# Kernel tuning notes

Measured on AMD Instinct MI355X. Metric: run time of the kernel, lower is better.

## Reference

```python
import jax, jax.numpy as jnp
from jax import lax
import numpy as np

S, B, HP, WP, CIN, CO, DS, DI, K = 6, 1, 37, 37, 1536, 256, 16, 512, 4
N = HP * WP          # 1369 patches (37x37 grid)
OH, OW = 148, 148
HID = max(S * CO // 4, S)  # 384, attention hidden


def setup_inputs() -> dict:
    key = jax.random.key(0)
    ks = iter(jax.random.split(key, 64))
    def nrm(shape, scale):
        return jax.random.normal(next(ks), shape, jnp.float32) * scale
    inp = {}
    inp["features"] = nrm((S, B, 1, N, CIN), 1.0)
    # AdaptiveFusionModule (global branch)
    inp["proj_w"] = nrm((S, CO, CIN), CIN ** -0.5)          # per-source 1x1 conv
    inp["attn_w1"] = nrm((S * CO, HID), (S * CO) ** -0.5)
    inp["attn_b1"] = jnp.zeros((HID,), jnp.float32)
    inp["attn_w2"] = nrm((HID, S), HID ** -0.5)
    inp["attn_b2"] = jnp.zeros((S,), jnp.float32)
    inp["src_scale"] = jnp.ones((S,), jnp.float32)
    # two SelectiveSSM parameter sets (fwd / bwd scan)
    def ssm_params(tag):
        d = {}
        d[tag + "_in_w"] = nrm((CO, 2 * DI), CO ** -0.5)
        d[tag + "_conv_w"] = nrm((K, DI), K ** -0.5)         # depthwise causal conv
        d[tag + "_conv_b"] = jnp.zeros((DI,), jnp.float32)
        d[tag + "_xp_w"] = nrm((DI, 2 * DS + DI + 1), 0.02)  # B, C, delta, dt_bias
        # trained A_log; scaled so the log-domain cumsum stays in fp32 range over L=1369
        d[tag + "_Alog"] = jnp.log(jnp.arange(1, DS + 1, dtype=jnp.float32) / 1000.0) * jnp.ones((DI, 1), jnp.float32)
        d[tag + "_D"] = jnp.ones((DI,), jnp.float32)
        d[tag + "_out_w"] = nrm((DI, CO), DI ** -0.5)
        d[tag + "_ln_g"] = jnp.ones((CO,), jnp.float32)
        d[tag + "_ln_b"] = jnp.zeros((CO,), jnp.float32)
        return d
    inp.update(ssm_params("f"))
    inp.update(ssm_params("b"))
    inp["merge_w"] = nrm((2 * CO, CO), (2 * CO) ** -0.5)     # MSSR merge 1x1 conv
    inp["co1_w"] = nrm((3, 3, CO, CO), (9 * CO) ** -0.5)     # conv_out1, HWIO
    inp["co1_b"] = jnp.zeros((CO,), jnp.float32)
    inp["hp"], inp["wp"], inp["out_h"], inp["out_w"] = HP, WP, OH, OW
    return inp


def _causal_dwconv(z, w, b):
    # z: [B,L,D], w: [K,D] -> torch Conv1d(groups=D, padding=K-1)[..., :L]
    Kk, L = w.shape[0], z.shape[1]
    zp = jnp.pad(z, ((0, 0), (Kk - 1, 0), (0, 0)))
    return sum(zp[:, k:k + L, :] * w[k] for k in range(Kk)) + b


def _ssm(x, in_w, conv_w, conv_b, xp_w, Alog, D, out_w, ln_g, ln_b):
    # x: [B,L,d_model] -> [B,L,d_model]
    z, gate = jnp.split(x @ in_w, 2, axis=-1)               # [B,L,DI] each
    z = jax.nn.silu(_causal_dwconv(z, conv_w, conv_b))
    xp = z @ xp_w                                           # [B,L,2*DS+DI+1]
    ds = Alog.shape[1]
    Bp, Cp = xp[..., :ds], xp[..., ds:2 * ds]
    delta = jax.nn.softplus(xp[..., 2 * ds:-1] + xp[..., -1:])  # [B,L,DI]
    dA = jnp.exp(delta[..., None] * (-jnp.exp(Alog)))       # [B,L,DI,DS]
    dBu = delta[..., None] * Bp[:, :, None, :] * z[..., None]
    # log-domain cumsum scan: h[t] = sum_s exp(cs[t]-cs[s]) * dBu[s]
    cs = jnp.cumsum(jnp.log(jnp.clip(dA, 1e-38)), axis=1)
    h = jnp.exp(cs) * jnp.cumsum(jnp.exp(-cs) * dBu, axis=1)
    y = (h * Cp[:, :, None, :]).sum(-1) + D * z             # [B,L,DI]
    y = (y * jax.nn.silu(gate)) @ out_w                     # [B,L,d_model]
    r = y + x                                               # residual + LayerNorm
    mu = r.mean(-1, keepdims=True)
    v = ((r - mu) ** 2).mean(-1, keepdims=True)
    return ln_g * (r - mu) * lax.rsqrt(v + 1e-5) + ln_b


def _forward(features, proj_w, attn_w1, attn_b1, attn_w2, attn_b2, src_scale,
             f_in_w, f_conv_w, f_conv_b, f_xp_w, f_Alog, f_D, f_out_w, f_ln_g, f_ln_b,
             b_in_w, b_conv_w, b_conv_b, b_xp_w, b_Alog, b_D, b_out_w, b_ln_g, b_ln_b,
             merge_w, co1_w, co1_b, hp, wp, out_h, out_w):
    feats = features[:, :, 0]                               # [S,B,N,Cin]
    pf = jnp.einsum('sbnc,soc->sbno', feats, proj_w)        # [S,B,N,Co] per-source 1x1 proj
    Bsz = pf.shape[1]
    concat = pf.mean(2).transpose(1, 0, 2).reshape(Bsz, -1)  # [B,S*Co] pooled concat
    w = jax.nn.softmax(jax.nn.relu(concat @ attn_w1 + attn_b1) @ attn_w2 + attn_b2, axis=-1)
    w = jax.nn.softmax(w * src_scale, axis=-1)              # double softmax as in torch
    fused = jnp.einsum('bs,sbnc->bnc', w, pf)               # [B,N,Co]
    # MSSR bidirectional scan over row-major flattened patches
    fwd = _ssm(fused, f_in_w, f_conv_w, f_conv_b, f_xp_w, f_Alog, f_D, f_out_w, f_ln_g, f_ln_b)
    bwd = _ssm(fused[:, ::-1], b_in_w, b_conv_w, b_conv_b, b_xp_w, b_Alog, b_D, b_out_w, b_ln_g, b_ln_b)[:, ::-1]
    out = jnp.concatenate([fwd, bwd], axis=-1) @ merge_w    # [B,N,Co]
    sp = out.reshape(Bsz, hp, wp, -1)                       # NHWC
    up = jax.image.resize(sp, (Bsz, out_h, out_w, sp.shape[-1]), method='bilinear')
    y = lax.conv_general_dilated(up, co1_w, (1, 1), 'SAME',
                                 dimension_numbers=('NHWC', 'HWIO', 'NHWC')) + co1_b
    return y.transpose(0, 3, 1, 2)                          # [B,Co,out_h,out_w]


def reference(features, proj_w, attn_w1, attn_b1, attn_w2, attn_b2, src_scale,
              f_in_w, f_conv_w, f_conv_b, f_xp_w, f_Alog, f_D, f_out_w, f_ln_g, f_ln_b,
              b_in_w, b_conv_w, b_conv_b, b_xp_w, b_Alog, b_D, b_out_w, b_ln_g, b_ln_b,
              merge_w, co1_w, co1_b, hp, wp, out_h, out_w):
    return _forward(features, proj_w, attn_w1, attn_b1, attn_w2, attn_b2, src_scale,
                    f_in_w, f_conv_w, f_conv_b, f_xp_w, f_Alog, f_D, f_out_w, f_ln_g, f_ln_b,
                    b_in_w, b_conv_w, b_conv_b, b_xp_w, b_Alog, b_D, b_out_w, b_ln_g, b_ln_b,
                    merge_w, co1_w, co1_b, hp, wp, out_h, out_w)
```

## Files before the change

### kernel.cpp

```cpp
#include <hip/hip_runtime.h>
#include <math.h>


namespace {
constexpr int kS   = 6;
constexpr int kHP  = 37;
constexpr int kWP  = 37;
constexpr int kN   = 1369;
constexpr int kCIN = 1536;
constexpr int kCO  = 256;
constexpr int kDS  = 16;
constexpr int kDI  = 512;
constexpr int kHID = 384;
constexpr int kOH  = 148;
constexpr int kOW  = 148;
constexpr int kNP  = kOH * kOW;
constexpr int kXPW = 545;
constexpr long kXPS = 746112;
constexpr int kNC  = 24;
constexpr int kCH  = 58;

constexpr long OFF_PF      = 0;
constexpr long OFF_Z2B     = 0;
constexpr long OFF_YGB     = 0;
constexpr long OFF_UPB     = 0;
constexpr long OFF_SCANP   = 700928;
constexpr long OFF_SCANH   = 1094144;
constexpr long OFF_HIN     = 1487360;
constexpr long OFF_OUTWT   = 1880576;
constexpr long OFF_COLPART = 2102784;
constexpr long OFF_WFIN    = 2119680;
constexpr long OFF_ATTNP   = 2119696;
constexpr long OFF_INWT    = 2200000;
constexpr long OFF_FUSEDB  = 2462144;
constexpr long OFF_ZG      = 2820624;
constexpr long OFF_Z       = 5760000;
constexpr long OFF_WCONVB  = 6000000;
constexpr long OFF_XP      = 7161856;
constexpr long OFF_DELTA   = 8654080;
constexpr long OFF_Y       = 10055936;
constexpr long OFF_GT      = 11457792;
constexpr long OFF_XPWT    = 11457792;
constexpr long OFF_FUSED2  = 12158720;
constexpr long OFF_CAT     = 12859648;
constexpr long OFF_MERGEWT = 13210112;
constexpr long OFF_MERGED  = 13560576;
}

typedef __attribute__((ext_vector_type(8))) short bf16x8;
typedef __attribute__((ext_vector_type(4))) float f32x4;

__device__ __forceinline__ short f2bf(float x) {
    unsigned u = __builtin_bit_cast(unsigned, x);
    unsigned r = u + 0x7fffu + ((u >> 16) & 1u);
    return (short)(r >> 16);
}

__device__ __forceinline__ bf16x8 cvt8(float4 x, float4 y) {
    union { short s[8]; bf16x8 v; } u;
    u.s[0] = f2bf(x.x); u.s[1] = f2bf(x.y); u.s[2] = f2bf(x.z); u.s[3] = f2bf(x.w);
    u.s[4] = f2bf(y.x); u.s[5] = f2bf(y.y); u.s[6] = f2bf(y.z); u.s[7] = f2bf(y.w);
    return u.v;
}

__global__ __launch_bounds__(256)
void transpose_cast_kernel(const float* __restrict__ w0, const float* __restrict__ w1,
                           short* __restrict__ wt, int K, int N)
{
    __shared__ float tile[32][33];
    int dir = blockIdx.z;
    const float* w = dir ? w1 : w0;
    short* o = wt + (long)dir * K * N;
    int k0 = blockIdx.x * 32, n0 = blockIdx.y * 32;
    int tx = threadIdx.x & 31, ty = threadIdx.x >> 5;
    #pragma unroll
    for (int r = 0; r < 32; r += 8) {
        int k = k0 + ty + r, n = n0 + tx;
        tile[ty + r][tx] = (k < K && n < N) ? w[(long)k * N + n] : 0.f;
    }
    __syncthreads();
    #pragma unroll
    for (int r = 0; r < 32; r += 8) {
        int n = n0 + ty + r, k = k0 + tx;
        if (n < N && k < K) o[(long)n * K + k] = f2bf(tile[tx][ty + r]);
    }
}

__global__ __launch_bounds__(256)
void mfma_nt(const short* __restrict__ A, long sA,
             const short* __restrict__ B, long sB,
             float* __restrict__ C, long sC,
             int M, int N, int K)
{
    __shared__ short smem[2][4096];
    const int bz = blockIdx.z;
    const short* Ab = A + (long)bz * sA;
    const short* Bb = B + (long)bz * sB;
    float* Cb = C + (long)bz * sC;
    const int t = threadIdx.x, w = t >> 6, l = t & 63;
    const int lr = l & 15, sg = l >> 4;
    const int m0 = blockIdx.x * 64, n0 = blockIdx.y * 64;

    const int row = t >> 2, qa = t & 3;
    int am = m0 + row; if (am >= M) am = M - 1;
    int bn = n0 + row; if (bn >= N) bn = N - 1;
    const long ga = (long)am * K + qa * 8;
    const long gb = (long)bn * K + qa * 8;
    const int woffA = row * 64 + ((qa ^ ((row >> 1) & 3)) << 4);
    const int woffB = 4096 + woffA;

    int aoff[2], boff[2];
    #pragma unroll
    for (int mi = 0; mi < 2; ++mi) {
        int r = (w >> 1) * 32 + mi * 16 + lr;
        aoff[mi] = r * 64 + ((sg ^ ((r >> 1) & 3)) << 4);
    }
    #pragma unroll
    for (int ni = 0; ni < 2; ++ni) {
        int r = (w & 1) * 32 + ni * 16 + lr;
        boff[ni] = 4096 + r * 64 + ((sg ^ ((r >> 1) & 3)) << 4);
    }

    f32x4 acc[2][2] = {};
    const int NT = K >> 5;
    {
        bf16x8 sa = *(const bf16x8*)(Ab + ga);
        bf16x8 sb = *(const bf16x8*)(Bb + gb);
        char* lb = (char*)&smem[0][0];
        *(bf16x8*)(lb + woffA) = sa;
        *(bf16x8*)(lb + woffB) = sb;
    }
    __syncthreads();
    for (int tt = 0; tt < NT; ++tt) {
        bf16x8 nsa, nsb;
        if (tt + 1 < NT) {
            long o = (long)(tt + 1) * 32;
            nsa = *(const bf16x8*)(Ab + ga + o);
            nsb = *(const bf16x8*)(Bb + gb + o);
        }
        char* lb = (char*)&smem[tt & 1][0];
        bf16x8 a[2], b[2];
        #pragma unroll
        for (int mi = 0; mi < 2; ++mi) a[mi] = *(const bf16x8*)(lb + aoff[mi]);
        #pragma unroll
        for (int ni = 0; ni < 2; ++ni) b[ni] = *(const bf16x8*)(lb + boff[ni]);
        #pragma unroll
        for (int mi = 0; mi < 2; ++mi)
            #pragma unroll
            for (int ni = 0; ni < 2; ++ni)
                acc[mi][ni] = __builtin_amdgcn_mfma_f32_16x16x32_bf16(a[mi], b[ni], acc[mi][ni], 0, 0, 0);
        if (tt + 1 < NT) {
            char* nb = (char*)&smem[(tt + 1) & 1][0];
            *(bf16x8*)(nb + woffA) = nsa;
            *(bf16x8*)(nb + woffB) = nsb;
        }
        __syncthreads();
    }
    const int q = l >> 4;
    const int wm0 = m0 + (w >> 1) * 32, wn0 = n0 + (w & 1) * 32;
    #pragma unroll
    for (int mi = 0; mi < 2; ++mi)
        #pragma unroll
        for (int ni = 0; ni < 2; ++ni)
            #pragma unroll
            for (int r = 0; r < 4; ++r) {
                int m = wm0 + mi * 16 + q * 4 + r;
                int n = wn0 + ni * 16 + lr;
                if (m < M && n < N)
                    Cb[(long)m * N + n] = acc[mi][ni][r];
            }
}

__global__ __launch_bounds__(256)
void proj_mfma_kernel(const float* __restrict__ Af, const float* __restrict__ Bf,
                      float* __restrict__ pf)
{
    __shared__ short smem[2][4096];
    const int s = blockIdx.z;
    const float* A = Af + (long)s * kN * kCIN;
    const float* B = Bf + (long)s * kCO * kCIN;
    float* C = pf + (long)s * kN * kCO;
    const int t = threadIdx.x, w = t >> 6, l = t & 63;
    const int lr = l & 15, sg = l >> 4;
    const int m0 = blockIdx.x * 64, n0 = blockIdx.y * 64;

    const int row = t >> 2, qa = t & 3;
    int am = m0 + row; if (am >= kN) am = kN - 1;
    const long ga = (long)am * kCIN + qa * 8;
    const long gb = (long)(n0 + row) * kCIN + qa * 8;
    const int woffA = row * 64 + ((qa ^ ((row >> 1) & 3)) << 4);
    const int woffB = 4096 + woffA;

    int aoff[2], boff[2];
    #pragma unroll
    for (int mi = 0; mi < 2; ++mi) {
        int r = (w >> 1) * 32 + mi * 16 + lr;
        aoff[mi] = r * 64 + ((sg ^ ((r >> 1) & 3)) << 4);
    }
    #pragma unroll
    for (int ni = 0; ni < 2; ++ni) {
        int r = (w & 1) * 32 + ni * 16 + lr;
        boff[ni] = 4096 + r * 64 + ((sg ^ ((r >> 1) & 3)) << 4);
    }

    f32x4 acc[2][2] = {};
    const int NT = kCIN >> 5;
    {
        float4 a0 = *(const float4*)(A + ga), a1 = *(const float4*)(A + ga + 4);
        float4 b0 = *(const float4*)(B + gb), b1 = *(const float4*)(B + gb + 4);
        char* lb = (char*)&smem[0][0];
        *(bf16x8*)(lb + woffA) = cvt8(a0, a1);
        *(bf16x8*)(lb + woffB) = cvt8(b0, b1);
    }
    __syncthreads();
    for (int tt = 0; tt < NT; ++tt) {
        float4 a0, a1, b0, b1;
        if (tt + 1 < NT) {
            long o = (long)(tt + 1) * 32;
            a0 = *(const float4*)(A + ga + o);     a1 = *(const float4*)(A + ga + o + 4);
            b0 = *(const float4*)(B + gb + o);     b1 = *(const float4*)(B + gb + o + 4);
        }
        char* lb = (char*)&smem[tt & 1][0];
        bf16x8 a[2], b[2];
        #pragma unroll
        for (int mi = 0; mi < 2; ++mi) a[mi] = *(const bf16x8*)(lb + aoff[mi]);
        #pragma unroll
        for (int ni = 0; ni < 2; ++ni) b[ni] = *(const bf16x8*)(lb + boff[ni]);
        #pragma unroll
        for (int mi = 0; mi < 2; ++mi)
            #pragma unroll
            for (int ni = 0; ni < 2; ++ni)
                acc[mi][ni] = __builtin_amdgcn_mfma_f32_16x16x32_bf16(a[mi], b[ni], acc[mi][ni], 0, 0, 0);
        if (tt + 1 < NT) {
            char* nb = (char*)&smem[(tt + 1) & 1][0];
            *(bf16x8*)(nb + woffA) = cvt8(a0, a1);
            *(bf16x8*)(nb + woffB) = cvt8(b0, b1);
        }
        __syncthreads();
    }
    const int q = l >> 4;
    const int wm0 = m0 + (w >> 1) * 32, wn0 = n0 + (w & 1) * 32;
    #pragma unroll
    for (int mi = 0; mi < 2; ++mi)
        #pragma unroll
        for (int ni = 0; ni < 2; ++ni)
            #pragma unroll
            for (int r = 0; r < 4; ++r) {
                int m = wm0 + mi * 16 + q * 4 + r;
                if (m < kN)
                    C[(long)m * kCO + wn0 + ni * 16 + lr] = acc[mi][ni][r];
            }
}

__global__ __launch_bounds__(256)
void conv_mfma_kernel(const short* __restrict__ up, const short* __restrict__ wt,
                      const float* __restrict__ bias, float* __restrict__ out)
{
    __shared__ short smem[2][6144];
    const int t = threadIdx.x, w = t >> 6, l = t & 63;
    const int lr = l & 15, sg = l >> 4;
    const int pm0 = blockIdx.x * 64;
    const int bn0 = blockIdx.y * 128;

    long gb[3]; int ldsoff[3]; int isA[3];
    #pragma unroll
    for (int i = 0; i < 3; ++i) {
        int j = w * 3 + i;
        int qa = l & 3;
        if (j < 4) {
            int row = j * 16 + (l >> 2);
            isA[i] = 1;
            int p = pm0 + row; if (p >= kNP) p = kNP - 1;
            int oy = p / kOW, ox = p - oy * kOW;
            gb[i] = ((long)oy * 150 + ox) * kCO + qa * 8;
            ldsoff[i] = row * 64 + ((qa ^ ((row >> 1) & 3)) << 4);
        } else {
            int row = (j - 4) * 16 + (l >> 2);
            isA[i] = 0;
            gb[i] = (long)(bn0 + row) * 2304 + qa * 8;
            ldsoff[i] = 4096 + row * 64 + ((qa ^ ((row >> 1) & 3)) << 4);
        }
    }
    int aoff[2], boff[4];
    #pragma unroll
    for (int mi = 0; mi < 2; ++mi) {
        int r = (w >> 1) * 32 + mi * 16 + lr;
        aoff[mi] = r * 64 + ((sg ^ ((r >> 1) & 3)) << 4);
    }
    #pragma unroll
    for (int ni = 0; ni < 4; ++ni) {
        int r = (w & 1) * 64 + ni * 16 + lr;
        boff[ni] = 4096 + r * 64 + ((sg ^ ((r >> 1) & 3)) << 4);
    }

    f32x4 acc[2][4] = {};
    const int NT = 72;
    {
        bf16x8 stg[3];
        #pragma unroll
        for (int i = 0; i < 3; ++i)
            stg[i] = isA[i] ? *(const bf16x8*)(up + gb[i])
                            : *(const bf16x8*)(wt + gb[i]);
        char* lb = (char*)&smem[0][0];
        #pragma unroll
        for (int i = 0; i < 3; ++i) *(bf16x8*)(lb + ldsoff[i]) = stg[i];
    }
    __syncthreads();

    for (int tt = 0; tt < NT; ++tt) {
        bf16x8 nstg[3];
        if (tt + 1 < NT) {
            int tn = tt + 1;
            int tap = tn >> 3, c0 = (tn & 7) << 5;
            int ky = tap / 3, kx = tap - ky * 3;
            long ta = ((long)ky * 150 + kx) * kCO + c0;
            long tb = (long)tn * 32;
            #pragma unroll
            for (int i = 0; i < 3; ++i)
                nstg[i] = isA[i] ? *(const bf16x8*)(up + gb[i] + ta)
                                 : *(const bf16x8*)(wt + gb[i] + tb);
        }
        char* lb = (char*)&smem[tt & 1][0];
        bf16x8 a[2], b[4];
        #pragma unroll
        for (int mi = 0; mi < 2; ++mi) a[mi] = *(const bf16x8*)(lb + aoff[mi]);
        #pragma unroll
        for (int ni = 0; ni < 4; ++ni) b[ni] = *(const bf16x8*)(lb + boff[ni]);
        #pragma unroll
        for (int mi = 0; mi < 2; ++mi)
            #pragma unroll
            for (int ni = 0; ni < 4; ++ni)
                acc[mi][ni] = __builtin_amdgcn_mfma_f32_16x16x32_bf16(a[mi], b[ni], acc[mi][ni], 0, 0, 0);
        if (tt + 1 < NT) {
            char* nb = (char*)&smem[(tt + 1) & 1][0];
            #pragma unroll
            for (int i = 0; i < 3; ++i) *(bf16x8*)(nb + ldsoff[i]) = nstg[i];
        }
        __syncthreads();
    }

    const int q = l >> 4;
    const int m0 = pm0 + (w >> 1) * 32;
    const int n0 = bn0 + (w & 1) * 64;
    #pragma unroll
    for (int mi = 0; mi < 2; ++mi)
        #pragma unroll
        for (int ni = 0; ni < 4; ++ni) {
            const int co = n0 + ni * 16 + lr;
            const float bv = bias[co];
            #pragma unroll
            for (int r = 0; r < 4; ++r) {
                int p = m0 + mi * 16 + q * 4 + r;
                if (p < kNP)
                    out[(long)co * kNP + p] = acc[mi][ni][r] + bv;
            }
        }
}

__global__ __launch_bounds__(256)
void colmean_kernel(const float* __restrict__ pf, float* __restrict__ colpart)
{
    int s = blockIdx.x, ch = blockIdx.y, o = threadIdx.x;
    int n0 = ch * 128, n1 = n0 + 128 > kN ? kN : n0 + 128;
    float a = 0.f;
    for (int n = n0; n < n1; ++n) a += pf[((long)s * kN + n) * kCO + o];
    colpart[ch * kS * kCO + s * kCO + o] = a;
}

__global__ __launch_bounds__(384)
void attn_part1(const float* __restrict__ colpart, const float* __restrict__ w1,
                float* __restrict__ partial)
{
    __shared__ float cm[128];
    int b = blockIdx.x, t = threadIdx.x;
    int c0 = b * 128;
    if (t < 128) {
        float a = 0.f;
        #pragma unroll
        for (int ch = 0; ch < 11; ++ch) a += colpart[ch * kS * kCO + c0 + t];
        cm[t] = a * (1.f / kN);
    }
    __syncthreads();
    float acc = 0.f;
    #pragma unroll 4
    for (int c = 0; c < 128; ++c) acc += cm[c] * w1[(long)(c0 + c) * kHID + t];
    partial[b * kHID + t] = acc;
}

__global__ __launch_bounds__(384)
void attn_part2(const float* __restrict__ partial, const float* __restrict__ b1,
                const float* __restrict__ w2, const float* __restrict__ b2,
                const float* __restrict__ ss, float* __restrict__ wfin)
{
    __shared__ float h[kHID];
    __shared__ float logits[8];
    int t = threadIdx.x;
    float acc = b1[t];
    #pragma unroll
    for (int b = 0; b < 12; ++b) acc += partial[b * kHID + t];
    h[t] = fmaxf(acc, 0.f);
    __syncthreads();
    if (t < kS) {
        float lg = b2[t];
        for (int j = 0; j < kHID; ++j) lg += h[j] * w2[j * kS + t];
        logits[t] = lg;
    }
    __syncthreads();
    if (t == 0) {
        float w[kS], mx = -1e30f, sum = 0.f;
        for (int s = 0; s < kS; ++s) mx = fmaxf(mx, logits[s]);
        for (int s = 0; s < kS; ++s) { w[s] = expf(logits[s] - mx); sum += w[s]; }
        for (int s = 0; s < kS; ++s) w[s] /= sum;
        mx = -1e30f;
        for (int s = 0; s < kS; ++s) { w[s] *= ss[s]; mx = fmaxf(mx, w[s]); }
        sum = 0.f;
        float e[kS];
        for (int s = 0; s < kS; ++s) { e[s] = expf(w[s] - mx); sum += e[s]; }
        for (int s = 0; s < kS; ++s) wfin[s] = e[s] / sum;
    }
}

__global__ __launch_bounds__(256)
void fuse_kernel(const float* __restrict__ pf, const float* __restrict__ wfin,
                 float* __restrict__ fused2, short* __restrict__ fusedb2)
{
    long idx = (long)blockIdx.x * 256 + threadIdx.x;
    if (idx >= (long)kN * kCO) return;
    float acc = 0.f;
    #pragma unroll
    for (int s = 0; s < kS; ++s) acc += wfin[s] * pf[(long)s * kN * kCO + idx];
    long n = idx / kCO; int c = (int)(idx % kCO);
    long ridx = (long)kN * kCO + (kN - 1 - n) * kCO + c;
    short bv = f2bf(acc);
    fused2[idx] = acc;
    fused2[ridx] = acc;
    fusedb2[idx] = bv;
    fusedb2[ridx] = bv;
}

__global__ __launch_bounds__(256)
void dwconv_kernel(const float* __restrict__ zg2,
                   const float* __restrict__ wf, const float* __restrict__ bf,
                   const float* __restrict__ wb, const float* __restrict__ bb,
                   float* __restrict__ z2, short* __restrict__ z2b)
{
    long idx = (long)blockIdx.x * 256 + threadIdx.x;
    int dir = blockIdx.y;
    if (idx >= (long)kN * kDI) return;
    long n = idx >> 9; int i = (int)(idx & (kDI - 1));
    const float* zg = zg2 + (long)dir * kN * 2 * kDI;
    const float* w  = dir ? wb : wf;
    const float* b  = dir ? bb : bf;
    float acc = b[i];
    #pragma unroll
    for (int k = 0; k < 4; ++k) {
        long m = n - 3 + k;
        if (m >= 0) acc += w[k * kDI + i] * zg[m * 2 * kDI + i];
    }
    float sg = 1.f / (1.f + expf(-acc));
    float v = acc * sg;
    z2 [(long)dir * kN * kDI + idx] = v;
    z2b[(long)dir * kN * kDI + idx] = f2bf(v);
}

__global__ __launch_bounds__(256)
void delta_kernel(const float* __restrict__ xp2, float* __restrict__ delta2)
{
    long idx = (long)blockIdx.x * 256 + threadIdx.x;
    int dir = blockIdx.y;
    if (idx >= (long)kN * kDI) return;
    long n = idx >> 9; int i = (int)(idx & (kDI - 1));
    const float* xp = xp2 + (long)dir * kXPS + n * kXPW;
    float x = xp[2 * kDS + i] + xp[kXPW - 1];
    float sp = fmaxf(x, 0.f) + log1pf(expf(-fabsf(x)));
    delta2[(long)dir * kN * kDI + idx] = sp;
}

__global__ __launch_bounds__(256)
void scan_partA(const float* __restrict__ delta2, const float* __restrict__ z2,
                const float* __restrict__ xp2,
                const float* __restrict__ Alogf, const float* __restrict__ Alogb,
                float* __restrict__ chunkP, float* __restrict__ chunkH)
{
    int bx = blockIdx.x;
    int c  = blockIdx.y;
    int dir = bx >> 5, iblk = bx & 31;
    int t = threadIdx.x;
    int s = t & 15, il = t >> 4;
    int i = iblk * 16 + il;
    int gid = dir * 8192 + iblk * 256 + t;
    const float* delta = delta2 + (long)dir * kN * kDI;
    const float* z     = z2     + (long)dir * kN * kDI;
    const float* xp    = xp2    + (long)dir * kXPS;
    const float* Alog  = dir ? Alogb : Alogf;
    float A = expf(Alog[i * kDS + s]);
    int n0 = c * kCH, n1 = n0 + kCH; if (n1 > kN) n1 = kN;
    float h = 0.f, P = 1.f;
    for (int n = n0; n < n1; ++n) {
        float dlt = delta[(long)n * kDI + i];
        float zv  = z[(long)n * kDI + i];
        float Bv  = xp[(long)n * kXPW + s];
        float dA  = __expf(-dlt * A);
        h = dA * h + dlt * Bv * zv;
        P *= dA;
    }
    chunkP[(long)c * 16384 + gid] = P;
    chunkH[(long)c * 16384 + gid] = h;
}

__global__ __launch_bounds__(256)
void scan_partB(const float* __restrict__ chunkP, const float* __restrict__ chunkH,
                float* __restrict__ hin)
{
    int gid = blockIdx.x * 256 + threadIdx.x;
    float H = 0.f;
    for (int c = 0; c < kNC; ++c) {
        hin[(long)c * 16384 + gid] = H;
        H = chunkP[(long)c * 16384 + gid] * H + chunkH[(long)c * 16384 + gid];
    }
}

__global__ __launch_bounds__(256)
void scan_partC(const float* __restrict__ delta2, const float* __restrict__ z2,
                const float* __restrict__ xp2,
                const float* __restrict__ Df, const float* __restrict__ Db,
                const float* __restrict__ Alogf, const float* __restrict__ Alogb,
                const float* __restrict__ hin, float* __restrict__ ybuf2)
{
    int bx = blockIdx.x;
    int c  = blockIdx.y;
    int dir = bx >> 5, iblk = bx & 31;
    int t = threadIdx.x;
    int s = t & 15, il = t >> 4;
    int i = iblk * 16 + il;
    int gid = dir * 8192 + iblk * 256 + t;
    const float* delta = delta2 + (long)dir * kN * kDI;
    const float* z     = z2     + (long)dir * kN * kDI;
    const float* xp    = xp2    + (long)dir * kXPS;
    const float* D     = dir ? Db : Df;
    const float* Alog  = dir ? Alogb : Alogf;
    float* y           = ybuf2  + (long)dir * kN * kDI;
    float A  = expf(Alog[i * kDS + s]);
    float Dv = D[i];
    int n0 = c * kCH, n1 = n0 + kCH; if (n1 > kN) n1 = kN;
    float h = hin[(long)c * 16384 + gid];
    for (int n = n0; n < n1; ++n) {
        float dlt = delta[(long)n * kDI + i];
        float zv  = z[(long)n * kDI + i];
        float Bv  = xp[(long)n * kXPW + s];
        float Cv  = xp[(long)n * kXPW + kDS + s];
        float dA  = __expf(-dlt * A);
        h = dA * h + dlt * Bv * zv;
        float cc = h * Cv;
        cc += __shfl_xor(cc, 1, 16);
        cc += __shfl_xor(cc, 2, 16);
        cc += __shfl_xor(cc, 4, 16);
        cc += __shfl_xor(cc, 8, 16);
        if (s == 0) y[(long)n * kDI + i] = cc + Dv * zv;
    }
}

__global__ __launch_bounds__(256)
void mulgate_kernel(const float* __restrict__ zg2, const float* __restrict__ ybuf2,
                    short* __restrict__ ygb)
{
    long idx = (long)blockIdx.x * 256 + threadIdx.x;
    int dir = blockIdx.y;
    if (idx >= (long)kN * kDI) return;
    long n = idx >> 9; int i = (int)(idx & (kDI - 1));
    float g = zg2[(long)dir * kN * 2 * kDI + n * 2 * kDI + kDI + i];
    float sg = 1.f / (1.f + expf(-g));
    float v = ybuf2[(long)dir * kN * kDI + idx] * g * sg;
    ygb[(long)dir * kN * kDI + idx] = f2bf(v);
}

__global__ __launch_bounds__(256)
void resid_ln_cat_kernel(const float* __restrict__ gt2, const float* __restrict__ x2,
                         const float* __restrict__ gf, const float* __restrict__ betf,
                         const float* __restrict__ gb, const float* __restrict__ betb,
                         short* __restrict__ catb)
{
    int n = blockIdx.x, dir = blockIdx.y, t = threadIdx.x;
    const float* gt = gt2 + ((long)dir * kN + n) * kCO;
    const float* x  = x2  + ((long)dir * kN + n) * kCO;
    const float* g  = dir ? gb : gf;
    const float* be = dir ? betb : betf;
    float r = gt[t] + x[t];
    float s1 = r, s2 = r * r;
    #pragma unroll
    for (int m = 32; m >= 1; m >>= 1) {
        s1 += __shfl_xor(s1, m, 64);
        s2 += __shfl_xor(s2, m, 64);
    }
    __shared__ float red[8];
    int w = t >> 6;
    if ((t & 63) == 0) { red[w] = s1; red[4 + w] = s2; }
    __syncthreads();
    float S1 = red[0] + red[1] + red[2] + red[3];
    float S2 = red[4] + red[5] + red[6] + red[7];
    float mu  = S1 * (1.f / kCO);
    float var = S2 * (1.f / kCO) - mu * mu;
    float inv = rsqrtf(var + 1e-5f);
    float v = g[t] * (r - mu) * inv + be[t];
    int row = dir ? (kN - 1 - n) : n;
    catb[(long)row * (2 * kCO) + dir * kCO + t] = f2bf(v);
}

__global__ __launch_bounds__(256)
void upsample_kernel(const float* __restrict__ merged, short* __restrict__ up)
{
    int p = blockIdx.x;
    int oy = p / kOW, ox = p - oy * kOW;
    int c = threadIdx.x;
    float sy = (oy + 0.5f) * ((float)kHP / (float)kOH) - 0.5f;
    float sx = (ox + 0.5f) * ((float)kWP / (float)kOW) - 0.5f;
    int iy0 = (int)floorf(sy); float fy = sy - (float)iy0;
    int ix0 = (int)floorf(sx); float fx = sx - (float)ix0;
    float wy0 = 1.f - fy, wy1 = fy, wx0 = 1.f - fx, wx1 = fx;
    int iy1 = iy0 + 1, ix1 = ix0 + 1;
    if (iy0 < 0)       { iy0 = 0;       wy0 = 0.f; }
    if (iy1 > kHP - 1) { iy1 = kHP - 1; wy1 = 0.f; }
    if (ix0 < 0)       { ix0 = 0;       wx0 = 0.f; }
    if (ix1 > kWP - 1) { ix1 = kWP - 1; wx1 = 0.f; }
    float wys = wy0 + wy1; wy0 /= wys; wy1 /= wys;
    float wxs = wx0 + wx1; wx0 /= wxs; wx1 /= wxs;
    const float* M00 = merged + (long)(iy0 * kWP + ix0) * kCO;
    const float* M01 = merged + (long)(iy0 * kWP + ix1) * kCO;
    const float* M10 = merged + (long)(iy1 * kWP + ix0) * kCO;
    const float* M11 = merged + (long)(iy1 * kWP + ix1) * kCO;
    float v = wy0 * (wx0 * M00[c] + wx1 * M01[c]) + wy1 * (wx0 * M10[c] + wx1 * M11[c]);
    up[((long)(oy + 1) * 150 + (ox + 1)) * kCO + c] = f2bf(v);
}

extern "C" void kernel_launch(void* const* d_in, const int* in_sizes, int n_in,
                              void* d_out, int out_size, void* d_ws, size_t ws_size,
                              hipStream_t stream)
{
    (void)in_sizes; (void)n_in; (void)out_size; (void)ws_size;
    const float* features  = (const float*)d_in[0];
    const float* proj_w    = (const float*)d_in[1];
    const float* attn_w1   = (const float*)d_in[2];
    const float* attn_b1   = (const float*)d_in[3];
    const float* attn_w2   = (const float*)d_in[4];
    const float* attn_b2   = (const float*)d_in[5];
    const float* src_scale = (const float*)d_in[6];
    const float* f_in_w    = (const float*)d_in[7];
    const float* f_conv_w  = (const float*)d_in[8];
    const float* f_conv_b  = (const float*)d_in[9];
    const float* f_xp_w    = (const float*)d_in[10];
    const float* f_Alog    = (const float*)d_in[11];
    const float* f_D       = (const float*)d_in[12];
    const float* f_out_w   = (const float*)d_in[13];
    const float* f_ln_g    = (const float*)d_in[14];
    const float* f_ln_b    = (const float*)d_in[15];
    const float* b_in_w    = (const float*)d_in[16];
    const float* b_conv_w  = (const float*)d_in[17];
    const float* b_conv_b  = (const float*)d_in[18];
    const float* b_xp_w    = (const float*)d_in[19];
    const float* b_Alog    = (const float*)d_in[20];
    const float* b_D       = (const float*)d_in[21];
    const float* b_out_w   = (const float*)d_in[22];
    const float* b_ln_g    = (const float*)d_in[23];
    const float* b_ln_b    = (const float*)d_in[24];
    const float* merge_w   = (const float*)d_in[25];
    const float* co1_w     = (const float*)d_in[26];
    const float* co1_b     = (const float*)d_in[27];

    float* ws      = (float*)d_ws;
    float* outp    = (float*)d_out;
    float* pf      = ws + OFF_PF;
    float* colpart = ws + OFF_COLPART;
    float* wfin    = ws + OFF_WFIN;
    float* attnp   = ws + OFF_ATTNP;
    float* fused2  = ws + OFF_FUSED2;
    float* zg2     = ws + OFF_ZG;
    float* z2      = ws + OFF_Z;
    float* xp2     = ws + OFF_XP;
    float* delta2  = ws + OFF_DELTA;
    float* ybuf2   = ws + OFF_Y;
    float* gt2     = ws + OFF_GT;
    float* merged  = ws + OFF_MERGED;
    float* chunkP  = ws + OFF_SCANP;
    float* chunkH  = ws + OFF_SCANH;
    float* hin     = ws + OFF_HIN;
    short* in_wt   = (short*)(ws + OFF_INWT);
    short* xp_wt   = (short*)(ws + OFF_XPWT);
    short* out_wt  = (short*)(ws + OFF_OUTWT);
    short* mrg_wt  = (short*)(ws + OFF_MERGEWT);
    short* fusedb2 = (short*)(ws + OFF_FUSEDB);
    short* z2b     = (short*)(ws + OFF_Z2B);
    short* ygb     = (short*)(ws + OFF_YGB);
    short* catb    = (short*)(ws + OFF_CAT);
    short* upb     = (short*)(ws + OFF_UPB);
    short* wconvb  = (short*)(ws + OFF_WCONVB);

    proj_mfma_kernel<<<dim3(22, 4, 6), 256, 0, stream>>>(features, proj_w, pf);
    transpose_cast_kernel<<<dim3(8, 32, 2), 256, 0, stream>>>(f_in_w, b_in_w, in_wt, 256, 1024);
    transpose_cast_kernel<<<dim3(16, 18, 2), 256, 0, stream>>>(f_xp_w, b_xp_w, xp_wt, 512, 545);
    transpose_cast_kernel<<<dim3(16, 8, 1), 256, 0, stream>>>(merge_w, merge_w, mrg_wt, 512, 256);
    colmean_kernel<<<dim3(6, 11), 256, 0, stream>>>(pf, colpart);
    attn_part1<<<dim3(12), 384, 0, stream>>>(colpart, attn_w1, attnp);
    attn_part2<<<1, 384, 0, stream>>>(attnp, attn_b1, attn_w2, attn_b2, src_scale, wfin);
    fuse_kernel<<<dim3(1369), 256, 0, stream>>>(pf, wfin, fused2, fusedb2);
    transpose_cast_kernel<<<dim3(16, 8, 2), 256, 0, stream>>>(f_out_w, b_out_w, out_wt, 512, 256);
    mfma_nt<<<dim3(22, 16, 2), 256, 0, stream>>>(
        fusedb2, (long)kN * kCO, in_wt, (long)2 * kDI * kCO,
        zg2, (long)kN * 2 * kDI, kN, 2 * kDI, kCO);
    dwconv_kernel<<<dim3(2738, 2), 256, 0, stream>>>(zg2, f_conv_w, f_conv_b,
                                                     b_conv_w, b_conv_b, z2, z2b);
    mfma_nt<<<dim3(22, 9, 2), 256, 0, stream>>>(
        z2b, (long)kN * kDI, xp_wt, (long)kXPW * kDI,
        xp2, kXPS, kN, kXPW, kDI);
    delta_kernel<<<dim3(2738, 2), 256, 0, stream>>>(xp2, delta2);
    scan_partA<<<dim3(64, kNC), 256, 0, stream>>>(delta2, z2, xp2, f_Alog, b_Alog,
                                                  chunkP, chunkH);
    scan_partB<<<dim3(64), 256, 0, stream>>>(chunkP, chunkH, hin);
    scan_partC<<<dim3(64, kNC), 256, 0, stream>>>(delta2, z2, xp2, f_D, b_D,
                                                  f_Alog, b_Alog, hin, ybuf2);
    mulgate_kernel<<<dim3(2738, 2), 256, 0, stream>>>(zg2, ybuf2, ygb);
    mfma_nt<<<dim3(22, 4, 2), 256, 0, stream>>>(
        ygb, (long)kN * kDI, out_wt, (long)kCO * kDI,
        gt2, (long)kN * kCO, kN, kCO, kDI);
    resid_ln_cat_kernel<<<dim3(1369, 2), 256, 0, stream>>>(gt2, fused2, f_ln_g, f_ln_b,
                                                           b_ln_g, b_ln_b, catb);
    mfma_nt<<<dim3(22, 4, 1), 256, 0, stream>>>(
        catb, 0, mrg_wt, 0,
        merged, 0, kN, kCO, 2 * kCO);
    transpose_cast_kernel<<<dim3(72, 8, 1), 256, 0, stream>>>(co1_w, co1_w, wconvb, 2304, 256);
    hipMemsetAsync(upb, 0, (size_t)150 * 150 * 256 * sizeof(short), stream);
    upsample_kernel<<<dim3(kNP), 256, 0, stream>>>(merged, upb);
    conv_mfma_kernel<<<dim3(343, 2), 256, 0, stream>>>(upb, wconvb, co1_b, outp);
}
```

Measured before the change: 316.1 us.

## Widen proj GEMM tiles to full N, remap blocks per XCD, deepen conv K-tile

The projection GEMM now has each block compute a 64x256 tile, covering all output channels, so the fp32 A rows are read and converted once instead of four times. The block index is remapped so consecutive work items land on the same XCD, which should help L2 locality. The conv GEMM K-step grows from 32 to 64 with a new 8-way LDS swizzle, halving the loop iterations and barriers. The cost is more registers and LDS per block and fewer blocks for the projection (132), which may lower occupancy and leave some CUs idle.

```diff
diff --git a/kernel.cpp b/kernel.cpp
--- a/kernel.cpp
+++ b/kernel.cpp
@@ -175,78 +175,97 @@
 void proj_mfma_kernel(const float* __restrict__ Af, const float* __restrict__ Bf,
                       float* __restrict__ pf)
 {
-    __shared__ short smem[2][4096];
-    const int s = blockIdx.z;
+    __shared__ short smem[2][10240];
+    const int bid = blockIdx.x;
+    const int xcd = bid & 7, slot = bid >> 3;
+    const int wid = (xcd < 4) ? xcd * 17 + slot : 68 + (xcd - 4) * 16 + slot;
+    const int s = wid / 22, mblk = wid - s * 22;
     const float* A = Af + (long)s * kN * kCIN;
     const float* B = Bf + (long)s * kCO * kCIN;
     float* C = pf + (long)s * kN * kCO;
+    const int m0 = mblk * 64;
+
     const int t = threadIdx.x, w = t >> 6, l = t & 63;
     const int lr = l & 15, sg = l >> 4;
-    const int m0 = blockIdx.x * 64, n0 = blockIdx.y * 64;
 
     const int row = t >> 2, qa = t & 3;
     int am = m0 + row; if (am >= kN) am = kN - 1;
     const long ga = (long)am * kCIN + qa * 8;
-    const long gb = (long)(n0 + row) * kCIN + qa * 8;
     const int woffA = row * 64 + ((qa ^ ((row >> 1) & 3)) << 4);
-    const int woffB = 4096 + woffA;
-
-    int aoff[2], boff[2];
-    #pragma unroll
-    for (int mi = 0; mi < 2; ++mi) {
-        int r = (w >> 1) * 32 + mi * 16 + lr;
+    long gb[4]; int woffB[4];
+    #pragma unroll
+    for (int j = 0; j < 4; ++j) {
+        int br = row + j * 64;
+        gb[j] = (long)br * kCIN + qa * 8;
+        woffB[j] = 4096 + br * 64 + ((qa ^ ((br >> 1) & 3)) << 4);
+    }
+
+    int aoff[4], boff[4];
+    #pragma unroll
+    for (int mi = 0; mi < 4; ++mi) {
+        int r = mi * 16 + lr;
         aoff[mi] = r * 64 + ((sg ^ ((r >> 1) & 3)) << 4);
     }
     #pragma unroll
-    for (int ni = 0; ni < 2; ++ni) {
-        int r = (w & 1) * 32 + ni * 16 + lr;
+    for (int ni = 0; ni < 4; ++ni) {
+        int r = w * 64 + ni * 16 + lr;
         boff[ni] = 4096 + r * 64 + ((sg ^ ((r >> 1) & 3)) << 4);
     }
 
-    f32x4 acc[2][2] = {};
+    f32x4 acc[4][4] = {};
     const int NT = kCIN >> 5;
     {
+        char* lb = (char*)&smem[0][0];
         float4 a0 = *(const float4*)(A + ga), a1 = *(const float4*)(A + ga + 4);
-        float4 b0 = *(const float4*)(B + gb), b1 = *(const float4*)(B + gb + 4);
-        char* lb = (char*)&smem[0][0];
         *(bf16x8*)(lb + woffA) = cvt8(a0, a1);
-        *(bf16x8*)(lb + woffB) = cvt8(b0, b1);
+        #pragma unroll
+        for (int j = 0; j < 4; ++j) {
+            float4 b0 = *(const float4*)(B + gb[j]), b1 = *(const float4*)(B + gb[j] + 4);
+            *(bf16x8*)(lb + woffB[j]) = cvt8(b0, b1);
+        }
     }
     __syncthreads();
     for (int tt = 0; tt < NT; ++tt) {
-        float4 a0, a1, b0, b1;
+        float4 na0, na1, nb0[4], nb1[4];
         if (tt + 1 < NT) {
             long o = (long)(tt + 1) * 32;
-            a0 = *(const float4*)(A + ga + o);     a1 = *(const float4*)(A + ga + o + 4);
-            b0 = *(const float4*)(B + gb + o);     b1 = *(const float4*)(B + gb + o + 4);
+            na0 = *(const float4*)(A + ga + o);
+            na1 = *(const float4*)(A + ga + o + 4);
+            #pragma unroll
+            for (int j = 0; j < 4; ++j) {
+                nb0[j] = *(const float4*)(B + gb[j] + o);
+                nb1[j] = *(const float4*)(B + gb[j] + o + 4);
+            }
         }
         char* lb = (char*)&smem[tt & 1][0];
-        bf16x8 a[2], b[2];
-        #pragma unroll
-        for (int mi = 0; mi < 2; ++mi) a[mi] = *(const bf16x8*)(lb + aoff[mi]);
-        #pragma unroll
-        for (int ni = 0; ni < 2; ++ni) b[ni] = *(const bf16x8*)(lb + boff[ni]);
-        #pragma unroll
-        for (int mi = 0; mi < 2; ++mi)
-            #pragma unroll
-            for (int ni = 0; ni < 2; ++ni)
+        bf16x8 a[4], b[4];
+        #pragma unroll
+        for (int mi = 0; mi < 4; ++mi) a[mi] = *(const bf16x8*)(lb + aoff[mi]);
+        #pragma unroll
+        for (int ni = 0; ni < 4; ++ni) b[ni] = *(const bf16x8*)(lb + boff[ni]);
+        #pragma unroll
+        for (int mi = 0; mi < 4; ++mi)
+            #pragma unroll
+            for (int ni = 0; ni < 4; ++ni)
                 acc[mi][ni] = __builtin_amdgcn_mfma_f32_16x16x32_bf16(a[mi], b[ni], acc[mi][ni], 0, 0, 0);
         if (tt + 1 < NT) {
             char* nb = (char*)&smem[(tt + 1) & 1][0];
-            *(bf16x8*)(nb + woffA) = cvt8(a0, a1);
-            *(bf16x8*)(nb + woffB) = cvt8(b0, b1);
+            *(bf16x8*)(nb + woffA) = cvt8(na0, na1);
+            #pragma unroll
+            for (int j = 0; j < 4; ++j)
+                *(bf16x8*)(nb + woffB[j]) = cvt8(nb0[j], nb1[j]);
         }
         __syncthreads();
     }
     const int q = l >> 4;
-    const int wm0 = m0 + (w >> 1) * 32, wn0 = n0 + (w & 1) * 32;
-    #pragma unroll
-    for (int mi = 0; mi < 2; ++mi)
-        #pragma unroll
-        for (int ni = 0; ni < 2; ++ni)
+    const int wn0 = w * 64;
+    #pragma unroll
+    for (int mi = 0; mi < 4; ++mi)
+        #pragma unroll
+        for (int ni = 0; ni < 4; ++ni)
             #pragma unroll
             for (int r = 0; r < 4; ++r) {
-                int m = wm0 + mi * 16 + q * 4 + r;
+                int m = m0 + mi * 16 + q * 4 + r;
                 if (m < kN)
                     C[(long)m * kCO + wn0 + ni * 16 + lr] = acc[mi][ni][r];
             }
@@ -256,85 +275,92 @@
 void conv_mfma_kernel(const short* __restrict__ up, const short* __restrict__ wt,
                       const float* __restrict__ bias, float* __restrict__ out)
 {
-    __shared__ short smem[2][6144];
+    __shared__ short smem[2][12288];
     const int t = threadIdx.x, w = t >> 6, l = t & 63;
     const int lr = l & 15, sg = l >> 4;
     const int pm0 = blockIdx.x * 64;
     const int bn0 = blockIdx.y * 128;
 
-    long gb[3]; int ldsoff[3]; int isA[3];
-    #pragma unroll
-    for (int i = 0; i < 3; ++i) {
-        int j = w * 3 + i;
-        int qa = l & 3;
-        if (j < 4) {
-            int row = j * 16 + (l >> 2);
-            isA[i] = 1;
-            int p = pm0 + row; if (p >= kNP) p = kNP - 1;
-            int oy = p / kOW, ox = p - oy * kOW;
-            gb[i] = ((long)oy * 150 + ox) * kCO + qa * 8;
-            ldsoff[i] = row * 64 + ((qa ^ ((row >> 1) & 3)) << 4);
-        } else {
-            int row = (j - 4) * 16 + (l >> 2);
-            isA[i] = 0;
-            gb[i] = (long)(bn0 + row) * 2304 + qa * 8;
-            ldsoff[i] = 4096 + row * 64 + ((qa ^ ((row >> 1) & 3)) << 4);
-        }
-    }
-    int aoff[2], boff[4];
+    const int srow = t >> 3, qa = t & 7;
+    long gA[2]; int woffA[2];
+    #pragma unroll
+    for (int j = 0; j < 2; ++j) {
+        int ar = srow + j * 32;
+        int p = pm0 + ar; if (p >= kNP) p = kNP - 1;
+        int oy = p / kOW, ox = p - oy * kOW;
+        gA[j] = ((long)oy * 150 + ox) * kCO + qa * 8;
+        woffA[j] = ar * 128 + ((qa ^ (ar & 7)) << 4);
+    }
+    long gB[4]; int woffB[4];
+    #pragma unroll
+    for (int j = 0; j < 4; ++j) {
+        int br = srow + j * 32;
+        gB[j] = (long)(bn0 + br) * 2304 + qa * 8;
+        woffB[j] = 8192 + br * 128 + ((qa ^ (br & 7)) << 4);
+    }
+
+    int aoff[2][2], boff[4][2];
     #pragma unroll
     for (int mi = 0; mi < 2; ++mi) {
         int r = (w >> 1) * 32 + mi * 16 + lr;
-        aoff[mi] = r * 64 + ((sg ^ ((r >> 1) & 3)) << 4);
+        #pragma unroll
+        for (int kk = 0; kk < 2; ++kk)
+            aoff[mi][kk] = r * 128 + (((kk * 4 + sg) ^ (r & 7)) << 4);
     }
     #pragma unroll
     for (int ni = 0; ni < 4; ++ni) {
         int r = (w & 1) * 64 + ni * 16 + lr;
-        boff[ni] = 4096 + r * 64 + ((sg ^ ((r >> 1) & 3)) << 4);
+        #pragma unroll
+        for (int kk = 0; kk < 2; ++kk)
+            boff[ni][kk] = 8192 + r * 128 + (((kk * 4 + sg) ^ (r & 7)) << 4);
     }
 
     f32x4 acc[2][4] = {};
-    const int NT = 72;
+    const int NT = 36;
     {
-        bf16x8 stg[3];
-        #pragma unroll
-        for (int i = 0; i < 3; ++i)
-            stg[i] = isA[i] ? *(const bf16x8*)(up + gb[i])
-                            : *(const bf16x8*)(wt + gb[i]);
         char* lb = (char*)&smem[0][0];
         #pragma unroll
-        for (int i = 0; i < 3; ++i) *(bf16x8*)(lb + ldsoff[i]) = stg[i];
+        for (int j = 0; j < 2; ++j)
+            *(bf16x8*)(lb + woffA[j]) = *(const bf16x8*)(up + gA[j]);
+        #pragma unroll
+        for (int j = 0; j < 4; ++j)
+            *(bf16x8*)(lb + woffB[j]) = *(const bf16x8*)(wt + gB[j]);
     }
     __syncthreads();
 
     for (int tt = 0; tt < NT; ++tt) {
-        bf16x8 nstg[3];
+        bf16x8 sa[2], sb[4];
         if (tt + 1 < NT) {
             int tn = tt + 1;
-            int tap = tn >> 3, c0 = (tn & 7) << 5;
+            int tap = tn >> 2, c0 = (tn & 3) << 6;
             int ky = tap / 3, kx = tap - ky * 3;
             long ta = ((long)ky * 150 + kx) * kCO + c0;
-            long tb = (long)tn * 32;
-            #pragma unroll
-            for (int i = 0; i < 3; ++i)
-                nstg[i] = isA[i] ? *(const bf16x8*)(up + gb[i] + ta)
-                                 : *(const bf16x8*)(wt + gb[i] + tb);
+            long tb = (long)tn * 64;
+            #pragma unroll
+            for (int j = 0; j < 2; ++j) sa[j] = *(const bf16x8*)(up + gA[j] + ta);
+            #pragma unroll
+            for (int j = 0; j < 4; ++j) sb[j] = *(const bf16x8*)(wt + gB[j] + tb);
         }
         char* lb = (char*)&smem[tt & 1][0];
-        bf16x8 a[2], b[4];
-        #pragma unroll
-        for (int mi = 0; mi < 2; ++mi) a[mi] = *(const bf16x8*)(lb + aoff[mi]);
-        #pragma unroll
-        for (int ni = 0; ni < 4; ++ni) b[ni] = *(const bf16x8*)(lb + boff[ni]);
-        #pragma unroll
-        for (int mi = 0; mi < 2; ++mi)
-            #pragma unroll
-            for (int ni = 0; ni < 4; ++ni)
-                acc[mi][ni] = __builtin_amdgcn_mfma_f32_16x16x32_bf16(a[mi], b[ni], acc[mi][ni], 0, 0, 0);
+        #pragma unroll
+        for (int kk = 0; kk < 2; ++kk) {
+            bf16x8 a[2], b[4];
+            #pragma unroll
+            for (int mi = 0; mi < 2; ++mi) a[mi] = *(const bf16x8*)(lb + aoff[mi][kk]);
+            #pragma unroll
+            for (int ni = 0; ni < 4; ++ni) b[ni] = *(const bf16x8*)(lb + boff[ni][kk]);
+            #pragma unroll
+            for (int mi = 0; mi < 2; ++mi)
+                #pragma unroll
+                for (int ni = 0; ni < 4; ++ni)
+                    acc[mi][ni] = __builtin_amdgcn_mfma_f32_16x16x32_bf16(a[mi], b[ni], acc[mi][ni], 0, 0, 0);
+        }
         if (tt + 1 < NT) {
             char* nb = (char*)&smem[(tt + 1) & 1][0];
             #pragma unroll
-            for (int i = 0; i < 3; ++i) *(bf16x8*)(nb + ldsoff[i]) = nstg[i];
+            for (int j = 0; j < 2; ++j) *(bf16x8*)(nb + woffA[j]) = sa[j];
+            #pragma unroll
+            for (int j = 0; j < 4; ++j) *(bf16x8*)(nb + woffB[j]) = sb[j];
         }
         __syncthreads();
     }
@@ -694,7 +720,7 @@
     short* upb     = (short*)(ws + OFF_UPB);
     short* wconvb  = (short*)(ws + OFF_WCONVB);
 
-    proj_mfma_kernel<<<dim3(22, 4, 6), 256, 0, stream>>>(features, proj_w, pf);
+    proj_mfma_kernel<<<dim3(132), 256, 0, stream>>>(features, proj_w, pf);
     transpose_cast_kernel<<<dim3(8, 32, 2), 256, 0, stream>>>(f_in_w, b_in_w, in_wt, 256, 1024);
     transpose_cast_kernel<<<dim3(16, 18, 2), 256, 0, stream>>>(f_xp_w, b_xp_w, xp_wt, 512, 545);
     transpose_cast_kernel<<<dim3(16, 8, 1), 256, 0, stream>>>(merge_w, merge_w, mrg_wt, 512, 256);
```

After: 310.9 us. No clear change (-1.6%).
